# Performance work log

Hardware: AMD Instinct MI355X
Metric: run time of the kernel (lower is better)

The kernel has to match this reference:

```python
import jax, jax.numpy as jnp
import numpy as np

C = 16          # scalar multiplicity of Rs_hidden = [(16, 0)]
NB = 10         # number_of_basis
H = 12          # radial MLP hidden size
MAX_R = 10.0
CENTERS = jnp.linspace(0.0, MAX_R, NB)
SIGMA = 0.8 * (MAX_R / (NB - 1))
GAUSS_NORM = 1.423085244900308   # e3nn GaussianRadialModel basis normalizer
Y0 = 1.0 / (2.0 * np.sqrt(np.pi))  # Y_{l=0} spherical harmonic constant


def setup_inputs() -> dict:
    key = jax.random.key(0)
    ks = jax.random.split(key, 9)
    z, n1, n2 = 4, 192, 192
    return {
        'input1': jax.random.normal(ks[0], (z, n1, C), jnp.float32),
        'input2': jax.random.normal(ks[1], (z, n2, C), jnp.float32),
        'xyz1': jax.random.normal(ks[2], (z, n1, 3), jnp.float32),
        'xyz2': jax.random.normal(ks[3], (z, n2, 3), jnp.float32),
        'mask': jax.random.randint(ks[4], (z, n1 + n2), 0, 2),
        'W_rad1': jax.random.normal(ks[5], (NB, H), jnp.float32),
        'W_rad_out': jax.random.normal(ks[6], (H, C * C), jnp.float32),
        'W_fc3': jax.random.normal(ks[7], (C, C), jnp.float32),
        'W_fc2': jax.random.normal(ks[8], (C, 1), jnp.float32),
    }


def _normalize(x, eps=1e-6):
    # torch .std defaults to unbiased (ddof=1)
    mean = x.mean(-1, keepdims=True)
    std = jnp.std(x, axis=-1, keepdims=True, ddof=1)
    return (x - mean) / (std + eps)


def reference(input1, input2, xyz1, xyz2, mask, W_rad1, W_rad_out, W_fc3, W_fc2):
    x = jnp.concatenate([input1, input2], axis=1)    # [z, n, C]
    xyz = jnp.concatenate([xyz1, xyz2], axis=1)      # [z, n, 3]
    z, n = x.shape[0], x.shape[1]

    # pairwise distances (eps keeps sqrt grad finite on the diagonal)
    diff = xyz[:, :, None, :] - xyz[:, None, :, :]   # [z, n, n, 3]
    d = jnp.sqrt(jnp.sum(diff * diff, axis=-1) + 1e-12)  # [z, n, n]

    # Gaussian radial basis + weight-normalized FC radial model (swish act)
    basis = jnp.exp(-jnp.square((d[..., None] - CENTERS) / SIGMA)) / GAUSS_NORM  # [z,n,n,NB]
    hmid = jax.nn.silu(basis @ W_rad1 / np.sqrt(NB))          # [z, n, n, H]
    R = hmid @ W_rad_out / np.sqrt(H)                         # [z, n, n, C*C]

    # l=0 TFN kernel: radial weights * Y_0 (trivial Clebsch-Gordan for scalars)
    K = R.reshape(z, n, n, C, C) * Y0                         # [z, a, b, i, j]
    y = jnp.einsum('zabij,zbj->zai', K, x)                    # [z, n, C]

    # Norm(Rs_hidden): per-irrep L2 norm; for scalars it's |x|
    y = jnp.abs(y)
    y = jnp.where(mask[..., None] == 0, 0.0, y)

    s = _normalize(jnp.sum(y, axis=1))                        # [z, C]
    h3 = jax.nn.leaky_relu(s @ W_fc3 / np.sqrt(C))            # fc3 + leaky_relu
    o = h3 @ W_fc2 / np.sqrt(C)                               # fc2
    return jax.nn.sigmoid(o).reshape(-1)                      # [z]
```

## Files before the change

### kernel.cpp

```cpp
#include <hip/hip_runtime.h>
#include <math.h>

#define Z     4
#define N1    192
#define NN    384
#define C     16
#define NB    10
#define H     12
#define ATILE 4
#define NAT   (NN / ATILE)
#define SPLIT 6

__device__ __forceinline__ float fexp2(float x) {
    float r; asm volatile("v_exp_f32 %0, %1" : "=v"(r) : "v"(x)); return r;
}
__device__ __forceinline__ float frcp(float x) {
    float r; asm volatile("v_rcp_f32 %0, %1" : "=v"(r) : "v"(x)); return r;
}

__device__ __forceinline__ float3 load_xyz(const float* __restrict__ xyz1,
                                           const float* __restrict__ xyz2,
                                           int z, int node) {
    const float* p = (node < N1) ? (xyz1 + (z * N1 + node) * 3)
                                 : (xyz2 + (z * N1 + (node - N1)) * 3);
    return make_float3(p[0], p[1], p[2]);
}

__global__ __launch_bounds__(384) void k1_precompute_T(const float* __restrict__ in1,
                                                       const float* __restrict__ in2,
                                                       const float* __restrict__ Wro,
                                                       float* __restrict__ T,
                                                       float* __restrict__ y_acc) {
    const int row = blockIdx.x;
    const int b   = threadIdx.x;
    const int z   = row / (H * C);
    const int hi  = row % (H * C);
    const int h   = hi >> 4, i = hi & 15;

    if (row < 64) y_acc[row * 384 + b] = 0.0f;

    const float* xp = (b < N1) ? (in1 + (z * N1 + b) * C)
                               : (in2 + (z * N1 + (b - N1)) * C);
    const float* w = Wro + h * (C * C) + i * C;
    const float4 x0 = *(const float4*)(xp + 0);
    const float4 x1 = *(const float4*)(xp + 4);
    const float4 x2 = *(const float4*)(xp + 8);
    const float4 x3 = *(const float4*)(xp + 12);
    float acc = 0.0f;
    acc += w[0]  * x0.x + w[1]  * x0.y + w[2]  * x0.z + w[3]  * x0.w;
    acc += w[4]  * x1.x + w[5]  * x1.y + w[6]  * x1.z + w[7]  * x1.w;
    acc += w[8]  * x2.x + w[9]  * x2.y + w[10] * x2.z + w[11] * x2.w;
    acc += w[12] * x3.x + w[13] * x3.y + w[14] * x3.z + w[15] * x3.w;

    const float scale = 0.28209479177387814f * 0.2886751345948129f;
    T[row * NN + b] = acc * scale;
}

__global__ __launch_bounds__(64) void k2_pairs(const float* __restrict__ xyz1,
                                               const float* __restrict__ xyz2,
                                               const float* __restrict__ Wr1,
                                               const float* __restrict__ T,
                                               float* __restrict__ y_acc) {
    const int bid = blockIdx.x;
    const int sp  = bid % SPLIT;
    const int za  = bid / SPLIT;
    const int z   = za / NAT, at = za % NAT;
    const int a0  = at * ATILE;
    const int lane = threadIdx.x;
    const int b = sp * 64 + lane;

    __shared__ float W1s[NB * H];
    for (int idx = lane; idx < NB * H; idx += 64)
        W1s[idx] = Wr1[idx] * (0.31622776601683794f * 0.7027283689263438f);
    __syncthreads();

    const float3 pb = load_xyz(xyz1, xyz2, z, b);

    float dd[ATILE];
    #pragma unroll
    for (int aa = 0; aa < ATILE; ++aa) {
        const float3 pa = load_xyz(xyz1, xyz2, z, a0 + aa);
        const float dx = pa.x - pb.x, dy = pa.y - pb.y, dz = pa.z - pb.z;
        dd[aa] = sqrtf(dx * dx + dy * dy + dz * dz + 1e-12f);
    }

    float hm[ATILE][H];
    #pragma unroll
    for (int aa = 0; aa < ATILE; ++aa)
        #pragma unroll
        for (int h = 0; h < H; ++h) hm[aa][h] = 0.0f;

    #pragma unroll
    for (int k = 0; k < NB; ++k) {
        const float4 w0 = *(const float4*)&W1s[k * H + 0];
        const float4 w1 = *(const float4*)&W1s[k * H + 4];
        const float4 w2 = *(const float4*)&W1s[k * H + 8];
        const float ck = (float)k * (10.0f / 9.0f);
        #pragma unroll
        for (int aa = 0; aa < ATILE; ++aa) {
            const float t = dd[aa] - ck;
            const float e = fexp2(t * t * -1.8259109111250943f);
            hm[aa][0]  += e * w0.x;  hm[aa][1]  += e * w0.y;
            hm[aa][2]  += e * w0.z;  hm[aa][3]  += e * w0.w;
            hm[aa][4]  += e * w1.x;  hm[aa][5]  += e * w1.y;
            hm[aa][6]  += e * w1.z;  hm[aa][7]  += e * w1.w;
            hm[aa][8]  += e * w2.x;  hm[aa][9]  += e * w2.y;
            hm[aa][10] += e * w2.z;  hm[aa][11] += e * w2.w;
        }
    }
    #pragma unroll
    for (int aa = 0; aa < ATILE; ++aa)
        #pragma unroll
        for (int h = 0; h < H; ++h) {
            const float x = hm[aa][h];
            const float sig = frcp(1.0f + fexp2(x * -1.4426950408889634f));
            hm[aa][h] = x * sig;
        }

    float v[ATILE * C];
    #pragma unroll
    for (int p = 0; p < ATILE * C; ++p) v[p] = 0.0f;

    const float* tb = T + (z * H * C) * NN + b;
    #pragma unroll
    for (int h = 0; h < H; ++h) {
        #pragma unroll
        for (int i = 0; i < C; ++i) {
            const float tval = tb[(h * C + i) * NN];
            #pragma unroll
            for (int aa = 0; aa < ATILE; ++aa)
                v[aa * C + i] += hm[aa][h] * tval;
        }
    }

    #pragma unroll
    for (int k = 0; k < 6; ++k) {
        const int m = 32 >> k;
        const int bsel = (lane >> k) & 1;
        #pragma unroll
        for (int j = 0; j < m; ++j) {
            const float lo = v[j], hi = v[m + j];
            const float sendv = bsel ? lo : hi;
            const float recv = __shfl_xor(sendv, 1 << k, 64);
            v[j] = (bsel ? hi : lo) + recv;
        }
    }
    const int l = lane;
    const int pos = ((l & 1) << 5) | ((l & 2) << 3) | ((l & 4) << 1) |
                    ((l & 8) >> 1) | ((l & 16) >> 3) | ((l & 32) >> 5);
    atomicAdd(&y_acc[(z * NN + a0) * C + pos], v[0]);
}

__global__ __launch_bounds__(256) void k3_head(const float* __restrict__ y_acc,
                                               const int* __restrict__ mask,
                                               const float* __restrict__ Wfc3,
                                               const float* __restrict__ Wfc2,
                                               float* __restrict__ out) {
    const int z = blockIdx.x;
    const int t = threadIdx.x;
    const int i = t & 15, ch = t >> 4;

    __shared__ float red[16][17];

    float acc = 0.0f;
    #pragma unroll
    for (int r = 0; r < 24; ++r) {
        const int a = ch * 24 + r;
        const float val = y_acc[(z * NN + a) * C + i];
        if (mask[z * NN + a] != 0) acc += fabsf(val);
    }
    red[ch][i] = acc;
    __syncthreads();

    if (t < C) {
        float x = 0.0f;
        #pragma unroll
        for (int c2 = 0; c2 < 16; ++c2) x += red[c2][t];

        float m = x;
        #pragma unroll
        for (int msk = 1; msk < 16; msk <<= 1) m += __shfl_xor(m, msk, 64);
        m *= (1.0f / 16.0f);
        const float dv = x - m;
        float vv = dv * dv;
        #pragma unroll
        for (int msk = 1; msk < 16; msk <<= 1) vv += __shfl_xor(vv, msk, 64);
        const float sd = sqrtf(vv / 15.0f) + 1e-6f;
        const float xn = dv / sd;

        float h3 = 0.0f;
        #pragma unroll
        for (int q = 0; q < 16; ++q)
            h3 += __shfl(xn, q, 64) * Wfc3[q * C + t];
        h3 *= 0.25f;
        h3 = (h3 > 0.0f) ? h3 : 0.01f * h3;

        float o = h3 * Wfc2[t];
        #pragma unroll
        for (int msk = 1; msk < 16; msk <<= 1) o += __shfl_xor(o, msk, 64);
        if (t == 0) out[z] = 1.0f / (1.0f + __expf(-0.25f * o));
    }
}

extern "C" void kernel_launch(void* const* d_in, const int* in_sizes, int n_in,
                              void* d_out, int out_size, void* d_ws, size_t ws_size,
                              hipStream_t stream) {
    const float* in1  = (const float*)d_in[0];
    const float* in2  = (const float*)d_in[1];
    const float* xyz1 = (const float*)d_in[2];
    const float* xyz2 = (const float*)d_in[3];
    const int*   mask = (const int*)d_in[4];
    const float* Wr1  = (const float*)d_in[5];
    const float* Wro  = (const float*)d_in[6];
    const float* Wfc3 = (const float*)d_in[7];
    const float* Wfc2 = (const float*)d_in[8];
    float* out = (float*)d_out;

    float* T     = (float*)d_ws;
    float* y_acc = T + Z * NN * H * C;

    k1_precompute_T<<<Z * H * C, 384, 0, stream>>>(in1, in2, Wro, T, y_acc);
    k2_pairs<<<Z * NAT * SPLIT, 64, 0, stream>>>(xyz1, xyz2, Wr1, T, y_acc);
    k3_head<<<Z, 256, 0, stream>>>(y_acc, mask, Wfc3, Wfc2, out);
}
```

Before: 95.36 us.

## Interleave T as float4 per lane for vectorized loads in pair kernel

```diff
diff --git a/kernel.cpp b/kernel.cpp
--- a/kernel.cpp
+++ b/kernel.cpp
@@ -31,29 +31,40 @@
                                                        const float* __restrict__ Wro,
                                                        float* __restrict__ T,
                                                        float* __restrict__ y_acc) {
-    const int row = blockIdx.x;
+    const int blk = blockIdx.x;
     const int b   = threadIdx.x;
-    const int z   = row / (H * C);
-    const int hi  = row % (H * C);
-    const int h   = hi >> 4, i = hi & 15;
-
-    if (row < 64) y_acc[row * 384 + b] = 0.0f;
+    const int ig  = blk & 3;
+    const int zh  = blk >> 2;
+    const int z   = zh / H, h = zh % H;
+    const int sp  = b >> 6, lane = b & 63;
+
+    if (blk < 64) y_acc[blk * 384 + b] = 0.0f;
 
     const float* xp = (b < N1) ? (in1 + (z * N1 + b) * C)
                                : (in2 + (z * N1 + (b - N1)) * C);
-    const float* w = Wro + h * (C * C) + i * C;
     const float4 x0 = *(const float4*)(xp + 0);
     const float4 x1 = *(const float4*)(xp + 4);
     const float4 x2 = *(const float4*)(xp + 8);
     const float4 x3 = *(const float4*)(xp + 12);
-    float acc = 0.0f;
-    acc += w[0]  * x0.x + w[1]  * x0.y + w[2]  * x0.z + w[3]  * x0.w;
-    acc += w[4]  * x1.x + w[5]  * x1.y + w[6]  * x1.z + w[7]  * x1.w;
-    acc += w[8]  * x2.x + w[9]  * x2.y + w[10] * x2.z + w[11] * x2.w;
-    acc += w[12] * x3.x + w[13] * x3.y + w[14] * x3.z + w[15] * x3.w;
 
     const float scale = 0.28209479177387814f * 0.2886751345948129f;
-    T[row * NN + b] = acc * scale;
+
+    float4 r;
+    float* rp = (float*)&r;
+    #pragma unroll
+    for (int c = 0; c < 4; ++c) {
+        const int i = ig * 4 + c;
+        const float* w = Wro + h * (C * C) + i * C;
+        float acc = 0.0f;
+        acc += w[0]  * x0.x + w[1]  * x0.y + w[2]  * x0.z + w[3]  * x0.w;
+        acc += w[4]  * x1.x + w[5]  * x1.y + w[6]  * x1.z + w[7]  * x1.w;
+        acc += w[8]  * x2.x + w[9]  * x2.y + w[10] * x2.z + w[11] * x2.w;
+        acc += w[12] * x3.x + w[13] * x3.y + w[14] * x3.z + w[15] * x3.w;
+        rp[c] = acc * scale;
+    }
+
+    float4* T4 = (float4*)T;
+    T4[(((z * SPLIT + sp) * H + h) * 4 + ig) * 64 + lane] = r;
 }
 
 __global__ __launch_bounds__(64) void k2_pairs(const float* __restrict__ xyz1,
@@ -121,15 +132,19 @@
     #pragma unroll
     for (int p = 0; p < ATILE * C; ++p) v[p] = 0.0f;
 
-    const float* tb = T + (z * H * C) * NN + b;
+    const float4* tb4 = (const float4*)T + ((z * SPLIT + sp) * H * 4) * 64 + lane;
     #pragma unroll
     for (int h = 0; h < H; ++h) {
         #pragma unroll
-        for (int i = 0; i < C; ++i) {
-            const float tval = tb[(h * C + i) * NN];
+        for (int ig = 0; ig < 4; ++ig) {
+            const float4 tv = tb4[(h * 4 + ig) * 64];
             #pragma unroll
-            for (int aa = 0; aa < ATILE; ++aa)
-                v[aa * C + i] += hm[aa][h] * tval;
+            for (int aa = 0; aa < ATILE; ++aa) {
+                const float f = hm[aa][h];
+                const int o = aa * C + ig * 4;
+                v[o + 0] += f * tv.x;  v[o + 1] += f * tv.y;
+                v[o + 2] += f * tv.z;  v[o + 3] += f * tv.w;
+            }
         }
     }
 
@@ -219,7 +234,7 @@
     float* T     = (float*)d_ws;
     float* y_acc = T + Z * NN * H * C;
 
-    k1_precompute_T<<<Z * H * C, 384, 0, stream>>>(in1, in2, Wro, T, y_acc);
+    k1_precompute_T<<<Z * H * 4, 384, 0, stream>>>(in1, in2, Wro, T, y_acc);
     k2_pairs<<<Z * NAT * SPLIT, 64, 0, stream>>>(xyz1, xyz2, Wr1, T, y_acc);
     k3_head<<<Z, 256, 0, stream>>>(y_acc, mask, Wfc3, Wfc2, out);
 }
```

New measurement: 94.16 us. No clear change (-1.3%).
